# Performance work log

Hardware: AMD Instinct MI355X
Metric: run time of the kernel (lower is better)

The kernel has to match this reference:

```python
import jax, jax.numpy as jnp
import numpy as np


def setup_inputs() -> dict:
    key = jax.random.key(0)
    ks = jax.random.split(key, 5)
    B, S, H = 4, 4096, 512
    std = 1.0 / np.sqrt(H)
    x = jax.random.normal(ks[0], (B, S, H), dtype=jnp.float32)
    relative_pos = jax.random.normal(ks[1], (B, S, H), dtype=jnp.float32)
    Wq = jax.random.normal(ks[2], (H, H), dtype=jnp.float32) * std
    Wk = jax.random.normal(ks[3], (H, H), dtype=jnp.float32) * std
    Wv = jax.random.normal(ks[4], (H, H), dtype=jnp.float32) * std
    bq = jnp.zeros((H,), dtype=jnp.float32)
    bk = jnp.zeros((H,), dtype=jnp.float32)
    bv = jnp.zeros((H,), dtype=jnp.float32)
    return {"x": x, "relative_pos": relative_pos, "Wq": Wq, "bq": bq,
            "Wk": Wk, "bk": bk, "Wv": Wv, "bv": bv}


def reference(x, relative_pos, Wq, bq, Wk, bk, Wv, bv):
    H = x.shape[-1]
    scale = jnp.sqrt(jnp.asarray(H, dtype=x.dtype))
    # torch Linear: y = x @ W^T + b
    Q = jnp.einsum('bsh,oh->bso', x, Wq) + bq
    K = jnp.einsum('bsh,oh->bso', x, Wk) + bk
    V = jnp.einsum('bsh,oh->bso', x, Wv) + bv
    Kr = jnp.einsum('bsh,oh->bso', relative_pos, Wk) + bk
    # two score terms, each [B,S,S]
    scores = (jnp.einsum('bqd,bkd->bqk', Q, K) +
              jnp.einsum('bqd,bkd->bqk', Q, Kr)) / scale
    weights = jax.nn.softmax(scores, axis=-1)
    return jnp.einsum('bqk,bkd->bqd', weights, V)
```

## Files before the change

### kernel.cpp

```cpp
#include <hip/hip_runtime.h>
#include <stdint.h>

typedef __attribute__((ext_vector_type(8))) short bf16x8;
typedef __attribute__((ext_vector_type(4))) float f32x4;

#define AS1 __attribute__((address_space(1)))
#define AS3 __attribute__((address_space(3)))

__device__ __forceinline__ void gl2lds16(const void* g, void* l) {
    __builtin_amdgcn_global_load_lds((const AS1 void*)g, (AS3 void*)l, 16, 0, 0);
}

__device__ __forceinline__ unsigned short f2bf(float f) {
    uint32_t u = __builtin_bit_cast(uint32_t, f);
    uint32_t r = (u + 0x7fffu + ((u >> 16) & 1u)) >> 16;
    return (unsigned short)r;
}

constexpr int S = 4096;
constexpr int H = 512;
constexpr size_t OFF_XB  = 0;
constexpr size_t OFF_SB  = 16777216;
constexpr size_t OFF_WQB = 33554432;
constexpr size_t OFF_WKB = 34078720;
constexpr size_t OFF_WVB = 34603008;
constexpr size_t OFF_BQK = 35127296;
constexpr size_t OFF_QB  = 35131392;
constexpr size_t OFF_K2B = OFF_QB  + 16777216;
constexpr size_t OFF_VTB = OFF_K2B + 16777216;
constexpr size_t OFF_PB  = OFF_VTB + 16777216;
constexpr size_t OFF_L   = OFF_PB  + 134217728;

__global__ __launch_bounds__(256) void prep_all(const float* __restrict__ x,
                                                const float* __restrict__ rp,
                                                const float* __restrict__ wq,
                                                const float* __restrict__ wk,
                                                const float* __restrict__ wv,
                                                const float* __restrict__ bq,
                                                const float* __restrict__ bk,
                                                unsigned short* __restrict__ xb,
                                                unsigned short* __restrict__ sb,
                                                unsigned short* __restrict__ wqb,
                                                unsigned short* __restrict__ wkb,
                                                unsigned short* __restrict__ wvb,
                                                float* __restrict__ bqk,
                                                float* __restrict__ lrow) {
    if (blockIdx.x < 8192) {
        const int i = (blockIdx.x * 256 + threadIdx.x) * 4;
        float4 xv = *(const float4*)(x + i);
        float4 rv = *(const float4*)(rp + i);
        uint2 xo, so;
        xo.x = (uint32_t)f2bf(xv.x) | ((uint32_t)f2bf(xv.y) << 16);
        xo.y = (uint32_t)f2bf(xv.z) | ((uint32_t)f2bf(xv.w) << 16);
        so.x = (uint32_t)f2bf(xv.x + rv.x) | ((uint32_t)f2bf(xv.y + rv.y) << 16);
        so.y = (uint32_t)f2bf(xv.z + rv.z) | ((uint32_t)f2bf(xv.w + rv.w) << 16);
        *(uint2*)(xb + i) = xo;
        *(uint2*)(sb + i) = so;
    } else {
        const int t = (blockIdx.x - 8192) * 256 + threadIdx.x;
        const int i = t * 4;
        float4 q = *(const float4*)(wq + i);
        float4 k = *(const float4*)(wk + i);
        float4 v = *(const float4*)(wv + i);
        uint2 o;
        o.x = (uint32_t)f2bf(q.x) | ((uint32_t)f2bf(q.y) << 16);
        o.y = (uint32_t)f2bf(q.z) | ((uint32_t)f2bf(q.w) << 16);
        *(uint2*)(wqb + i) = o;
        o.x = (uint32_t)f2bf(k.x) | ((uint32_t)f2bf(k.y) << 16);
        o.y = (uint32_t)f2bf(k.z) | ((uint32_t)f2bf(k.w) << 16);
        *(uint2*)(wkb + i) = o;
        o.x = (uint32_t)f2bf(v.x) | ((uint32_t)f2bf(v.y) << 16);
        o.y = (uint32_t)f2bf(v.z) | ((uint32_t)f2bf(v.w) << 16);
        *(uint2*)(wvb + i) = o;
        if (t < 128) {
            *(float4*)(bqk + t * 4) = *(const float4*)(bq + t * 4);
        } else if (t < 256) {
            const int u = t - 128;
            float4 b = *(const float4*)(bk + u * 4);
            *(float4*)(bqk + 512 + u * 4) = make_float4(2.f * b.x, 2.f * b.y, 2.f * b.z, 2.f * b.w);
        }
        if (t < 4096) {
            *(float4*)(lrow + t * 4) = make_float4(0.f, 0.f, 0.f, 0.f);
        }
    }
}

template <int MODE, int SWZ, int NPANEL>
__global__ __launch_bounds__(256, 2)
void gemm_bt(const unsigned short* __restrict__ Abase,
             const unsigned short* __restrict__ Bbase,
             void* __restrict__ Cbase,
             int M, int N, int K,
             long long sAz, long long sBz, long long sCz,
             const float* __restrict__ bias_n, long long sBNz,
             const float* __restrict__ bias_m,
             float scale,
             float* __restrict__ rowdiv, long long sRz)
{
    int bx = blockIdx.x, by = blockIdx.y, bz = blockIdx.z;
    if (SWZ) {
        const int gx = gridDim.x, gy = gridDim.y;
        const int id  = bx + gx * (by + gridDim.y * bz);
        const int xcd = id & 7;
        const int k   = id >> 3;
        const int kg  = k / gx;
        bx = k - kg * gx;
        const int g = xcd + 8 * kg;
        const int gz = g / gy;
        by = g - gz * gy;
        bz = gz;
    }
    const int z = bz;
    const unsigned short* A  = Abase + (size_t)z * (size_t)sAz;
    const unsigned short* Bm = Bbase + (size_t)z * (size_t)sBz;
    const int bn = bx * 128;
    const int bm = by * 128;

    constexpr int STAGE_BYTES = NPANEL * 16384;
    constexpr int SMEM_BYTES = (MODE == 1) ? STAGE_BYTES
                             : (STAGE_BYTES > 34816 ? STAGE_BYTES : 34816);
    __shared__ __align__(16) char smem[SMEM_BYTES];
    unsigned short* As = (unsigned short*)smem;
    unsigned short* Bs = (unsigned short*)(smem + NPANEL * 8192);

    const int tid  = threadIdx.x;
    const int wave = tid >> 6;
    const int lane = tid & 63;
    const int lm   = lane & 15;
    const int quad = lane >> 4;
    const int wm   = (wave >> 1) * 64;
    const int wn   = (wave & 1) * 64;

    const int r0 = tid >> 2;
    const int p0 = tid & 3;

    f32x4 acc[4][4] = {};

    for (int k0 = 0; k0 < K; k0 += 32 * NPANEL) {
        __syncthreads();
        #pragma unroll
        for (int pp = 0; pp < NPANEL; pp++) {
            const unsigned short* Ap = A  + (size_t)(bm + r0) * K + k0 + pp * 32 + p0 * 8;
            const unsigned short* Bp = Bm + (size_t)(bn + r0) * K + k0 + pp * 32 + p0 * 8;
            unsigned short* Asp = As + pp * 4096;
            unsigned short* Bsp = Bs + pp * 4096;
            gl2lds16(Ap,                    Asp + wave * 512);
            gl2lds16(Ap + (size_t)64 * K,   Asp + 2048 + wave * 512);
            gl2lds16(Bp,                    Bsp + wave * 512);
            gl2lds16(Bp + (size_t)64 * K,   Bsp + 2048 + wave * 512);
        }
        __syncthreads();

        #pragma unroll
        for (int pp = 0; pp < NPANEL; pp++) {
            bf16x8 af[4], bfr[4];
            #pragma unroll
            for (int t = 0; t < 4; t++)
                af[t]  = *(const bf16x8*)(As + pp * 4096 + (wm + t * 16 + lm) * 32 + quad * 8);
            #pragma unroll
            for (int t = 0; t < 4; t++)
                bfr[t] = *(const bf16x8*)(Bs + pp * 4096 + (wn + t * 16 + lm) * 32 + quad * 8);
            #pragma unroll
            for (int mt = 0; mt < 4; mt++)
                #pragma unroll
                for (int nt = 0; nt < 4; nt++)
                    acc[mt][nt] = __builtin_amdgcn_mfma_f32_16x16x32_bf16(af[mt], bfr[nt], acc[mt][nt], 0, 0, 0);
        }
    }

    if (MODE == 1) {
        float* C = (float*)Cbase + (size_t)z * (size_t)sCz;
        const float* rd = rowdiv + (size_t)z * (size_t)sRz;
        #pragma unroll
        for (int mt = 0; mt < 4; mt++) {
            #pragma unroll
            for (int i = 0; i < 4; i++) {
                const int row = bm + wm + mt * 16 + quad * 4 + i;
                const float inv = 1.0f / rd[row];
                const size_t rb = (size_t)row * (size_t)N;
                #pragma unroll
                for (int nt = 0; nt < 4; nt++) {
                    const int col = bn + wn + nt * 16 + lm;
                    C[rb + col] = acc[mt][nt][i] * inv;
                }
            }
        }
    } else {
        unsigned short* C = (unsigned short*)Cbase + (size_t)z * (size_t)sCz;
        const float* bn_ptr = (MODE == 0 && bias_n) ? bias_n + (size_t)z * (size_t)sBNz : nullptr;
        float* lr = (MODE == 2) ? rowdiv + (size_t)z * (size_t)sRz : nullptr;
        unsigned short* Ct = (unsigned short*)smem;
        __syncthreads();
        #pragma unroll
        for (int mt = 0; mt < 4; mt++) {
            #pragma unroll
            for (int i = 0; i < 4; i++) {
                const int r = wm + mt * 16 + quad * 4 + i;
                if (MODE == 0) {
                    const float badd = bias_m ? bias_m[bm + r] : 0.0f;
                    #pragma unroll
                    for (int nt = 0; nt < 4; nt++) {
                        const int col = bn + wn + nt * 16 + lm;
                        float v = acc[mt][nt][i] * scale + badd;
                        if (bn_ptr) v += bn_ptr[col];
                        Ct[r * 136 + wn + nt * 16 + lm] = f2bf(v);
                    }
                } else {
                    float rsum = 0.f;
                    #pragma unroll
                    for (int nt = 0; nt < 4; nt++) {
                        float p = __expf(acc[mt][nt][i] * scale);
                        rsum += p;
                        Ct[r * 136 + wn + nt * 16 + lm] = f2bf(p);
                    }
                    rsum += __shfl_xor(rsum, 1);
                    rsum += __shfl_xor(rsum, 2);
                    rsum += __shfl_xor(rsum, 4);
                    rsum += __shfl_xor(rsum, 8);
                    if (lm == 0) atomicAdd(lr + bm + r, rsum);
                }
            }
        }
        __syncthreads();
        #pragma unroll
        for (int j = 0; j < 8; j++) {
            const int r   = (tid >> 4) + 16 * j;
            const int c16 = tid & 15;
            uint4 vv = *(const uint4*)(Ct + r * 136 + c16 * 8);
            *(uint4*)(C + (size_t)(bm + r) * (size_t)N + bn + c16 * 8) = vv;
        }
    }
}

__global__ __launch_bounds__(512, 2)
void qk_exp_8ph(const unsigned short* __restrict__ Qb,
                const unsigned short* __restrict__ K2b,
                unsigned short* __restrict__ Pb,
                float* __restrict__ lrow)
{
    constexpr int N  = 4096;
    constexpr int Kd = 512;
    constexpr float scale = 0.044194173824159216f;
    __shared__ __align__(16) char smem8[131072];

    int bx = blockIdx.x, by = blockIdx.y, bz = blockIdx.z;
    {
        const int gx = gridDim.x, gy = gridDim.y;
        const int id  = bx + gx * (by + gy * bz);
        const int xcd = id & 7;
        const int k   = id >> 3;
        const int kg  = k / gx;
        bx = k - kg * gx;
        const int g = xcd + 8 * kg;
        const int gz = g / gy;
        by = g - gz * gy;
        bz = gz;
    }
    const int z  = bz;
    const int bm = by * 256;
    const int bn = bx * 256;
    const unsigned short* Az = Qb  + (size_t)z * (size_t)N * Kd;
    const unsigned short* Bz = K2b + (size_t)z * (size_t)N * Kd;

    unsigned short* A0 = (unsigned short*)smem8;
    unsigned short* B0 = A0 + 256 * 64;
    unsigned short* A1 = B0 + 256 * 64;
    unsigned short* B1 = A1 + 256 * 64;

    const int tid  = threadIdx.x;
    const int wave = tid >> 6;
    const int lane = tid & 63;
    const int lm   = lane & 15;
    const int quad = lane >> 4;
    const int r2   = wave >> 2;
    const int c4   = wave & 3;

    const int srcslot = (lane & 7) ^ ((lane >> 3) & 7);
    const unsigned short* aSt = Az + (size_t)(bm + wave * 16 + (lane >> 3)) * Kd + srcslot * 8;
    const unsigned short* bSt = Bz + (size_t)(bn + wave * 16 + (lane >> 3)) * Kd + srcslot * 8;
    unsigned short* aLd0 = A0 + wave * 16 * 64;
    unsigned short* bLd0 = B0 + wave * 16 * 64;
    unsigned short* aLd1 = A1 + wave * 16 * 64;
    unsigned short* bLd1 = B1 + wave * 16 * 64;

#define STG(gbase, ld, t, h) { \
    gl2lds16((gbase) + (h) * 128 * Kd + (t) * 64,          (ld) + (h) * 128 * 64); \
    gl2lds16((gbase) + (h) * 128 * Kd + 8 * Kd + (t) * 64, (ld) + (h) * 128 * 64 + 8 * 64); }

    f32x4 acc[2][2][4][2] = {};
    bf16x8 af[4][2], bf0[2][2], bf1[2][2];

#define LD_AF(Abuf, HM) { _Pragma("unroll") for (int m = 0; m < 4; ++m) { \
      const int row_ = (HM) * 128 + r2 * 64 + m * 16 + lm; \
      const char* rp_ = (const char*)(Abuf) + row_ * 128; \
      const int sw_ = (row_ & 7) << 4; \
      af[m][0] = *(const bf16x8*)(rp_ + ((quad * 16) ^ sw_)); \
      af[m][1] = *(const bf16x8*)(rp_ + ((64 + quad * 16) ^ sw_)); } }

#define LD_BF(dst, Bbuf, HN) { _Pragma("unroll") for (int n = 0; n < 2; ++n) { \
      const int row_ = (HN) * 128 + c4 * 32 + n * 16 + lm; \
      const char* rp_ = (const char*)(Bbuf) + row_ * 128; \
      const int sw_ = (row_ & 7) << 4; \
      dst[n][0] = *(const bf16x8*)(rp_ + ((quad * 16) ^ sw_)); \
      dst[n][1] = *(const bf16x8*)(rp_ + ((64 + quad * 16) ^ sw_)); } }

#define MM(HM, HN, BF) { _Pragma("unroll") for (int m = 0; m < 4; ++m) \
      _Pragma("unroll") for (int n = 0; n < 2; ++n) \
      _Pragma("unroll") for (int ks = 0; ks < 2; ++ks) \
        acc[HM][HN][m][n] = __builtin_amdgcn_mfma_f32_16x16x32_bf16(af[m][ks], BF[n][ks], acc[HM][HN][m][n], 0, 0, 0); }

#define BAR_MFMA(HM, HN, BF) \
    __builtin_amdgcn_s_barrier(); \
    asm volatile("s_waitcnt lgkmcnt(0)" ::: "memory"); \
    __builtin_amdgcn_sched_barrier(0); \
    __builtin_amdgcn_s_setprio(1); \
    MM(HM, HN, BF); \
    __builtin_amdgcn_s_setprio(0);

    STG(aSt, aLd0, 0, 0); STG(aSt, aLd0, 0, 1);
    STG(bSt, bLd0, 0, 0); STG(bSt, bLd0, 0, 1);
    STG(aSt, aLd1, 1, 0);
    STG(bSt, bLd1, 1, 0);
    asm volatile("s_waitcnt vmcnt(4)" ::: "memory");
    __builtin_amdgcn_s_barrier();

    #pragma unroll
    for (int i = 0; i < 4; ++i) {
        const int t1 = 2 * i + 1, t2 = 2 * i + 2, t3 = 2 * i + 3;
        LD_AF(A0, 0); LD_BF(bf0, B0, 0);
        STG(aSt, aLd1, t1, 1); STG(bSt, bLd1, t1, 1);
        BAR_MFMA(0, 0, bf0);
        __builtin_amdgcn_s_barrier();
        LD_BF(bf1, B0, 1);
        BAR_MFMA(0, 1, bf1);
        __builtin_amdgcn_s_barrier();
        LD_AF(A0, 1);
        if (t2 < 8) STG(aSt, aLd0, t2, 0);
        BAR_MFMA(1, 0, bf0);
        __builtin_amdgcn_s_barrier();
        if (t2 < 8) STG(bSt, bLd0, t2, 0);
        BAR_MFMA(1, 1, bf1);
        if (i == 3) { asm volatile("s_waitcnt vmcnt(0)" ::: "memory"); }
        else        { asm volatile("s_waitcnt vmcnt(4)" ::: "memory"); }
        __builtin_amdgcn_s_barrier();
        LD_AF(A1, 0); LD_BF(bf0, B1, 0);
        if (t2 < 8) { STG(aSt, aLd0, t2, 1); STG(bSt, bLd0, t2, 1); }
        BAR_MFMA(0, 0, bf0);
        __builtin_amdgcn_s_barrier();
        LD_BF(bf1, B1, 1);
        BAR_MFMA(0, 1, bf1);
        __builtin_amdgcn_s_barrier();
        LD_AF(A1, 1);
        if (t3 < 8) STG(aSt, aLd1, t3, 0);
        BAR_MFMA(1, 0, bf0);
        __builtin_amdgcn_s_barrier();
        if (t3 < 8) STG(bSt, bLd1, t3, 0);
        BAR_MFMA(1, 1, bf1);
        asm volatile("s_waitcnt vmcnt(4)" ::: "memory");
        __builtin_amdgcn_s_barrier();
    }

    asm volatile("" ::: "memory");
    unsigned short* Ct = (unsigned short*)smem8;
    float* lr = lrow + (size_t)z * 4096;
    unsigned short* Cz = Pb + (size_t)z * (size_t)N * N;

    #pragma unroll
    for (int hm = 0; hm < 2; ++hm)
    #pragma unroll
    for (int m = 0; m < 4; ++m)
    #pragma unroll
    for (int i2 = 0; i2 < 4; ++i2) {
        const int row = hm * 128 + r2 * 64 + m * 16 + quad * 4 + i2;
        char* rowp = (char*)Ct + row * 512;
        const int sw = (row & 7) << 4;
        float rs = 0.f;
        #pragma unroll
        for (int hn = 0; hn < 2; ++hn)
        #pragma unroll
        for (int n = 0; n < 2; ++n) {
            const float p = __expf(acc[hm][hn][m][n][i2] * scale);
            rs += p;
            const int col = hn * 128 + c4 * 32 + n * 16 + lm;
            *(unsigned short*)(rowp + ((col * 2) ^ sw)) = f2bf(p);
        }
        rs += __shfl_xor(rs, 1);
        rs += __shfl_xor(rs, 2);
        rs += __shfl_xor(rs, 4);
        rs += __shfl_xor(rs, 8);
        if (lm == 0) atomicAdd(lr + bm + row, rs);
    }
    asm volatile("s_waitcnt lgkmcnt(0)" ::: "memory");
    __builtin_amdgcn_s_barrier();
    __builtin_amdgcn_sched_barrier(0);
    #pragma unroll
    for (int j = 0; j < 16; ++j) {
        const int row = j * 16 + (tid >> 5);
        const int cg  = tid & 31;
        const uint4 v = *(const uint4*)((const char*)Ct + row * 512 + ((cg * 16) ^ ((row & 7) << 4)));
        *(uint4*)(Cz + (size_t)(bm + row) * N + bn + cg * 8) = v;
    }
#undef STG
#undef LD_AF
#undef LD_BF
#undef MM
#undef BAR_MFMA
}

extern "C" void kernel_launch(void* const* d_in, const int* in_sizes, int n_in,
                              void* d_out, int out_size, void* d_ws, size_t ws_size,
                              hipStream_t stream) {
    const float* x  = (const float*)d_in[0];
    const float* rp = (const float*)d_in[1];
    const float* Wq = (const float*)d_in[2];
    const float* bq = (const float*)d_in[3];
    const float* Wk = (const float*)d_in[4];
    const float* bk = (const float*)d_in[5];
    const float* Wv = (const float*)d_in[6];
    const float* bv = (const float*)d_in[7];

    char* ws = (char*)d_ws;
    unsigned short* xb  = (unsigned short*)(ws + OFF_XB);
    unsigned short* sb  = (unsigned short*)(ws + OFF_SB);
    unsigned short* wqb = (unsigned short*)(ws + OFF_WQB);
    unsigned short* wkb = (unsigned short*)(ws + OFF_WKB);
    unsigned short* wvb = (unsigned short*)(ws + OFF_WVB);
    float*          bqk = (float*)(ws + OFF_BQK);
    unsigned short* qb  = (unsigned short*)(ws + OFF_QB);
    unsigned short* k2b = (unsigned short*)(ws + OFF_K2B);
    unsigned short* vtb = (unsigned short*)(ws + OFF_VTB);
    unsigned short* pb  = (unsigned short*)(ws + OFF_PB);
    float*          lrow = (float*)(ws + OFF_L);

    prep_all<<<8448, 256, 0, stream>>>(x, rp, Wq, Wk, Wv, bq, bk,
                                       xb, sb, wqb, wkb, wvb, bqk, lrow);

    gemm_bt<0, 1, 2><<<dim3(4, 128, 2), 256, 0, stream>>>(
        xb, wqb, qb, 16384, 512, 512,
        8388608, 262144, 8388608,
        bqk, 512, nullptr, 1.0f, nullptr, 0);
    gemm_bt<0, 0, 2><<<dim3(32, 4, 4), 256, 0, stream>>>(
        wvb, xb, vtb, 512, 4096, 512,
        0, (long long)S * H, (long long)S * H,
        nullptr, 0, bv, 1.0f, nullptr, 0);
    qk_exp_8ph<<<dim3(16, 16, 4), 512, 0, stream>>>(qb, k2b, pb, lrow);
    gemm_bt<1, 1, 4><<<dim3(4, 32, 4), 256, 0, stream>>>(
        pb, vtb, d_out, 4096, 512, 4096,
        (long long)S * S, (long long)S * H, (long long)S * H,
        nullptr, 0, nullptr, 1.0f, lrow, 4096);
}
```

Before: 357.2 us.

## Restructure score GEMM main loop into per-tile double-buffer with fewer barriers

Replaces the finely interleaved staging schedule, which had a barrier around each of four MFMA sub-blocks per K tile, with a simpler per-tile body. Each tile issues the full global-to-LDS prefetch of the next tile up front, then loads fragments and runs the four MFMA sub-blocks separated only by lgkmcnt waits, and ends with one vmcnt wait and one barrier. This is meant to cut barrier and synchronisation overhead per K step. In exchange, prefetch issue is less spread across compute and each tile ends on a full vmcnt(0) wait, which could expose more memory latency.

```diff
diff --git a/kernel.cpp b/kernel.cpp
--- a/kernel.cpp
+++ b/kernel.cpp
@@ -287,6 +287,10 @@
     gl2lds16((gbase) + (h) * 128 * Kd + (t) * 64,          (ld) + (h) * 128 * 64); \
     gl2lds16((gbase) + (h) * 128 * Kd + 8 * Kd + (t) * 64, (ld) + (h) * 128 * 64 + 8 * 64); }
 
+#define STG_TILE(ald, bld, t) { \
+    STG(aSt, ald, t, 0); STG(aSt, ald, t, 1); \
+    STG(bSt, bld, t, 0); STG(bSt, bld, t, 1); }
+
     f32x4 acc[2][2][4][2] = {};
     bf16x8 af[4][2], bf0[2][2], bf1[2][2];
 
@@ -309,55 +313,37 @@
       _Pragma("unroll") for (int ks = 0; ks < 2; ++ks) \
         acc[HM][HN][m][n] = __builtin_amdgcn_mfma_f32_16x16x32_bf16(af[m][ks], BF[n][ks], acc[HM][HN][m][n], 0, 0, 0); }
 
-#define BAR_MFMA(HM, HN, BF) \
-    __builtin_amdgcn_s_barrier(); \
+    STG_TILE(aLd0, bLd0, 0);
+    asm volatile("s_waitcnt vmcnt(0)" ::: "memory");
+    __builtin_amdgcn_s_barrier();
+
+#define TILE_BODY(T, AB, BB, ALD_O, BLD_O) { \
+    if ((T) + 1 < 8) { STG_TILE(ALD_O, BLD_O, (T) + 1); } \
+    LD_AF(AB, 0); LD_BF(bf0, BB, 0); LD_BF(bf1, BB, 1); \
+    asm volatile("s_waitcnt lgkmcnt(4)" ::: "memory"); \
+    __builtin_amdgcn_sched_barrier(0); \
+    __builtin_amdgcn_s_setprio(1); \
+    MM(0, 0, bf0); \
+    __builtin_amdgcn_s_setprio(0); \
     asm volatile("s_waitcnt lgkmcnt(0)" ::: "memory"); \
     __builtin_amdgcn_sched_barrier(0); \
     __builtin_amdgcn_s_setprio(1); \
-    MM(HM, HN, BF); \
-    __builtin_amdgcn_s_setprio(0);
-
-    STG(aSt, aLd0, 0, 0); STG(aSt, aLd0, 0, 1);
-    STG(bSt, bLd0, 0, 0); STG(bSt, bLd0, 0, 1);
-    STG(aSt, aLd1, 1, 0);
-    STG(bSt, bLd1, 1, 0);
-    asm volatile("s_waitcnt vmcnt(4)" ::: "memory");
-    __builtin_amdgcn_s_barrier();
+    MM(0, 1, bf1); \
+    __builtin_amdgcn_s_setprio(0); \
+    LD_AF(AB, 1); \
+    asm volatile("s_waitcnt lgkmcnt(0)" ::: "memory"); \
+    __builtin_amdgcn_sched_barrier(0); \
+    __builtin_amdgcn_s_setprio(1); \
+    MM(1, 0, bf0); \
+    MM(1, 1, bf1); \
+    __builtin_amdgcn_s_setprio(0); \
+    if ((T) + 1 < 8) { asm volatile("s_waitcnt vmcnt(0)" ::: "memory"); } \
+    __builtin_amdgcn_s_barrier(); }
 
     #pragma unroll
-    for (int i = 0; i < 4; ++i) {
-        const int t1 = 2 * i + 1, t2 = 2 * i + 2, t3 = 2 * i + 3;
-        LD_AF(A0, 0); LD_BF(bf0, B0, 0);
-        STG(aSt, aLd1, t1, 1); STG(bSt, bLd1, t1, 1);
-        BAR_MFMA(0, 0, bf0);
-        __builtin_amdgcn_s_barrier();
-        LD_BF(bf1, B0, 1);
-        BAR_MFMA(0, 1, bf1);
-        __builtin_amdgcn_s_barrier();
-        LD_AF(A0, 1);
-        if (t2 < 8) STG(aSt, aLd0, t2, 0);
-        BAR_MFMA(1, 0, bf0);
-        __builtin_amdgcn_s_barrier();
-        if (t2 < 8) STG(bSt, bLd0, t2, 0);
-        BAR_MFMA(1, 1, bf1);
-        if (i == 3) { asm volatile("s_waitcnt vmcnt(0)" ::: "memory"); }
-        else        { asm volatile("s_waitcnt vmcnt(4)" ::: "memory"); }
-        __builtin_amdgcn_s_barrier();
-        LD_AF(A1, 0); LD_BF(bf0, B1, 0);
-        if (t2 < 8) { STG(aSt, aLd0, t2, 1); STG(bSt, bLd0, t2, 1); }
-        BAR_MFMA(0, 0, bf0);
-        __builtin_amdgcn_s_barrier();
-        LD_BF(bf1, B1, 1);
-        BAR_MFMA(0, 1, bf1);
-        __builtin_amdgcn_s_barrier();
-        LD_AF(A1, 1);
-        if (t3 < 8) STG(aSt, aLd1, t3, 0);
-        BAR_MFMA(1, 0, bf0);
-        __builtin_amdgcn_s_barrier();
-        if (t3 < 8) STG(bSt, bLd1, t3, 0);
-        BAR_MFMA(1, 1, bf1);
-        asm volatile("s_waitcnt vmcnt(4)" ::: "memory");
-        __builtin_amdgcn_s_barrier();
+    for (int tp = 0; tp < 4; ++tp) {
+        TILE_BODY(2 * tp,     A0, B0, aLd1, bLd1);
+        TILE_BODY(2 * tp + 1, A1, B1, aLd0, bLd0);
     }
 
     asm volatile("" ::: "memory");
@@ -401,10 +387,11 @@
         *(uint4*)(Cz + (size_t)(bm + row) * N + bn + cg * 8) = v;
     }
 #undef STG
+#undef STG_TILE
 #undef LD_AF
 #undef LD_BF
 #undef MM
-#undef BAR_MFMA
+#undef TILE_BODY
 }
 
 extern "C" void kernel_launch(void* const* d_in, const int* in_sizes, int n_in,
```

Result: no change. 363.9 us (+1.9%).
